# Kernel optimization log

Measured on AMD Instinct MI355X. Metric: run time of the kernel, lower is better.

Reference implementation:

```python
import jax, jax.numpy as jnp
import numpy as np

DIM = 64      # d_model, expand=1 -> d_inner = DIM
H_IN = 128
W_IN = 128
DS = 8        # d_state
DTR = 4       # dt_rank = ceil(DIM/16)
DCONV = 4     # conv kernel size
NDIR = 4      # bimamba v6: h-fwd, h-bwd, w-fwd, w-bwd


def layernorm(x, g, b, eps=1e-5):
    m = x.mean(-1, keepdims=True)
    v = x.var(-1, keepdims=True)
    return (x - m) / jnp.sqrt(v + eps) * g + b


def causal_conv(x, w, b):
    # x: (B, L, D), w: (D, 1, K) depthwise, causal left pad
    xt = x.transpose(0, 2, 1)  # (B, D, L)
    y = jax.lax.conv_general_dilated(xt, w, (1,), [(DCONV - 1, 0)],
                                     feature_group_count=xt.shape[1])
    return y.transpose(0, 2, 1) + b


def selective_scan(u, delta, A, Bm, Cm, D):
    # u,delta: (B,L,D); A: (D,N); Bm,Cm: (B,L,N); D: (D,)
    dA = jnp.exp(delta[..., None] * A)                       # (B,L,D,N)
    dBu = delta[..., None] * Bm[:, :, None, :] * u[..., None]

    def comb(c1, c2):
        a1, b1 = c1
        a2, b2 = c2
        return a1 * a2, a2 * b1 + b2

    _, hs = jax.lax.associative_scan(comb, (dA, dBu), axis=1)  # (B,L,D,N)
    return jnp.einsum('bldn,bln->bld', hs, Cm) + u * D


def setup_inputs() -> dict:
    key = jax.random.key(0)
    ks = jax.random.split(key, 12)
    s = 0.02
    inp = {
        'input': jax.random.normal(ks[0], (2, DIM, H_IN, W_IN), jnp.float32),
        'ln_g': jnp.ones((DIM,), jnp.float32),
        'ln_b': jnp.zeros((DIM,), jnp.float32),
        'in_proj_w': jax.random.normal(ks[1], (2 * DIM, DIM), jnp.float32) * s,
        'conv_w': jax.random.normal(ks[2], (NDIR, DIM, 1, DCONV), jnp.float32) * s,
        'conv_b': jnp.zeros((NDIR, DIM), jnp.float32),
        'xproj_w': jax.random.normal(ks[3], (NDIR, DTR + 2 * DS, DIM), jnp.float32) * s,
        'dtproj_w': jax.random.normal(ks[4], (NDIR, DIM, DTR), jnp.float32) * s,
        'dtproj_b': jax.random.normal(ks[5], (NDIR, DIM), jnp.float32) * 0.1,
        'A_log': jnp.broadcast_to(jnp.log(jnp.arange(1.0, DS + 1.0, dtype=jnp.float32)),
                                  (NDIR, DIM, DS)).copy(),
        'D_skip': jnp.ones((NDIR, DIM), jnp.float32),
        'on_g': jnp.ones((DIM,), jnp.float32),
        'on_b': jnp.zeros((DIM,), jnp.float32),
        'out_proj_w': jax.random.normal(ks[6], (DIM, DIM), jnp.float32) * s,
    }
    return inp


def reference(input, ln_g, ln_b, in_proj_w, conv_w, conv_b, xproj_w,
              dtproj_w, dtproj_b, A_log, D_skip, on_g, on_b, out_proj_w):
    B, C, H, W = input.shape
    L = H * W
    seq = input.reshape(B, C, L).transpose(0, 2, 1)           # b (h w) c
    seq = layernorm(seq, ln_g, ln_b)
    xz = seq @ in_proj_w.T                                    # (B,L,2D)
    x, z = jnp.split(xz, 2, axis=-1)

    ar = jnp.arange(L)
    perm = (ar % H) * W + ar // H    # (h w) -> (w h)
    inv = (ar % W) * H + ar // W     # (w h) -> (h w)

    dirs = [(None, False), (None, True), (perm, False), (perm, True)]
    y_sum = jnp.zeros_like(x)
    for i, (p, rev) in enumerate(dirs):
        xd = x if p is None else x[:, p]
        if rev:
            xd = jnp.flip(xd, 1)
        xd = jax.nn.silu(causal_conv(xd, conv_w[i], conv_b[i]))
        dbl = xd @ xproj_w[i].T
        dt, Bm, Cm = jnp.split(dbl, [DTR, DTR + DS], axis=-1)
        dt = jax.nn.softplus(dt @ dtproj_w[i].T + dtproj_b[i])
        A = -jnp.exp(A_log[i])
        yd = selective_scan(xd, dt, A, Bm, Cm, D_skip[i])
        if rev:
            yd = jnp.flip(yd, 1)
        if p is not None:
            yd = yd[:, inv]
        y_sum = y_sum + yd

    y = y_sum / float(NDIR)                 # if_devide_out=True
    y = layernorm(y, on_g, on_b)            # use_norm=True
    y = y * jax.nn.silu(z)                  # gate
    out = y @ out_proj_w.T
    return out.transpose(0, 2, 1).reshape(B, C, H, W) + input
```

## Files before the change

### kernel.cpp

```cpp
#include <hip/hip_runtime.h>
#include <hip/hip_bf16.h>
#include <cstdint>
#include <cstddef>

#define L_TOT 16384
#define B_SZ 2
#define NROW (B_SZ * L_TOT)
#define CHUNK 32
#define NCH (L_TOT / CHUNK)

static constexpr size_t SLOT_XD  = (size_t)NROW * 64;
static constexpr size_t SLOT_DBC = (size_t)NROW * 20;
static constexpr size_t SLOT_SDT = (size_t)B_SZ * 64 * NCH;
static constexpr size_t SLOT_HC  = (size_t)B_SZ * NCH * 64 * 8;

__device__ __forceinline__ int tau_map(int dir, int s) {
  int j = (dir & 1) ? (L_TOT - 1 - s) : s;
  if (dir >= 2) j = ((j & 127) << 7) | (j >> 7);
  return j;
}
__device__ __forceinline__ float silu_f(float x) { return x / (1.f + __expf(-x)); }
__device__ __forceinline__ float softplus_f(float x) {
  return fmaxf(x, 0.f) + __logf(1.f + __expf(-fabsf(x)));
}

__global__ void __launch_bounds__(256)
k_ln_inproj(const float* __restrict__ inp, const float* __restrict__ lng,
            const float* __restrict__ lnb, const float* __restrict__ W,
            float* __restrict__ xout, float* __restrict__ zout) {
  __shared__ float xt[64 * 65];
  __shared__ float wrk[8448];
  const int t = threadIdx.x;
  const int lane = t & 63;
  const int w = t >> 6;
  const int b = blockIdx.x >> 8;
  const int l0 = (blockIdx.x & 255) << 6;
  const float* ip = inp + (size_t)b * 64 * L_TOT + l0 + lane;
#pragma unroll 4
  for (int cc = 0; cc < 16; ++cc) {
    int c = cc * 4 + w;
    xt[lane * 65 + c] = ip[(size_t)c * L_TOT];
  }
  __syncthreads();
  {
    float s1 = 0.f, s2 = 0.f;
    const int c0 = w * 16;
#pragma unroll
    for (int cc = 0; cc < 16; ++cc) {
      float v = xt[lane * 65 + c0 + cc];
      s1 += v; s2 = fmaf(v, v, s2);
    }
    wrk[w * 64 + lane] = s1;
    wrk[256 + w * 64 + lane] = s2;
  }
  __syncthreads();
  if (t < 64) {
    float s1 = wrk[t] + wrk[64 + t] + wrk[128 + t] + wrk[192 + t];
    float s2 = wrk[256 + t] + wrk[320 + t] + wrk[384 + t] + wrk[448 + t];
    float m = s1 * 0.015625f;
    float var = s2 * 0.015625f - m * m;
    wrk[512 + t] = m;
    wrk[576 + t] = rsqrtf(var + 1e-5f);
  }
  __syncthreads();
  {
    const float mv = wrk[512 + lane], rv = wrk[576 + lane];
#pragma unroll 4
    for (int k = 0; k < 16; ++k) {
      int c = w + 4 * k;
      float g = lng[c], bb = lnb[c];
      float v = xt[lane * 65 + c];
      xt[lane * 65 + c] = (v - mv) * rv * g + bb;
    }
  }
  __syncthreads();
#pragma unroll 4
  for (int rep = 0; rep < 32; ++rep) {
    int j = rep * 4 + w;
    wrk[j * 65 + lane] = W[(size_t)j * 64 + lane];
  }
  __syncthreads();
  const int rg = lane & 15;
  const int jg = lane >> 4;
  const int j0 = w * 32 + jg * 8;
  const int r0 = rg * 4;
  float acc[4][8] = {};
#pragma unroll 2
  for (int c = 0; c < 64; ++c) {
    float xv[4], wv[8];
#pragma unroll
    for (int i = 0; i < 4; ++i) xv[i] = xt[(r0 + i) * 65 + c];
#pragma unroll
    for (int jj = 0; jj < 8; ++jj) wv[jj] = wrk[(j0 + jj) * 65 + c];
#pragma unroll
    for (int i = 0; i < 4; ++i)
#pragma unroll
      for (int jj = 0; jj < 8; ++jj) acc[i][jj] = fmaf(xv[i], wv[jj], acc[i][jj]);
  }
  __syncthreads();
#pragma unroll
  for (int i = 0; i < 4; ++i)
#pragma unroll
    for (int jj = 0; jj < 8; ++jj) wrk[(r0 + i) * 132 + j0 + jj] = acc[i][jj];
  __syncthreads();
  float* xo = xout + ((size_t)b * L_TOT + l0) * 64;
  float* zo = zout + ((size_t)b * L_TOT + l0) * 64;
#pragma unroll 4
  for (int rep = 0; rep < 16; ++rep) {
    int r = rep * 4 + w;
    xo[(size_t)r * 64 + lane] = wrk[r * 132 + lane];
    zo[(size_t)r * 64 + lane] = wrk[r * 132 + 64 + lane];
  }
}

__global__ void __launch_bounds__(256)
k_convproj(const float* __restrict__ xbuf, const float* __restrict__ cw,
           const float* __restrict__ cb, const float* __restrict__ xpw,
           float* __restrict__ xd_base, float* __restrict__ dbc_base,
           int dir_base) {
  __shared__ float xh[67 * 65];
  __shared__ float wt[20 * 65];
  __shared__ float dbl[64 * 20];
  const int t = threadIdx.x;
  const int lane = t & 63;
  const int w = t >> 6;
  const int slot = blockIdx.y;
  const int dir = dir_base + slot;
  const int blk = blockIdx.x;
  const int b = blk >> 8;
  const int s0 = (blk & 255) << 6;
  const float* xb = xbuf + (size_t)b * L_TOT * 64;
#pragma unroll 1
  for (int i = w; i < 67; i += 4) {
    int s = s0 - 3 + i;
    float v = 0.f;
    if (s >= 0) v = xb[(size_t)tau_map(dir, s) * 64 + lane];
    xh[i * 65 + lane] = v;
  }
#pragma unroll
  for (int jj = 0; jj < 5; ++jj) {
    int j = jj * 4 + w;
    wt[j * 65 + lane] = xpw[((size_t)dir * 20 + j) * 64 + lane];
  }
  __syncthreads();
  float wk[4];
#pragma unroll
  for (int k = 0; k < 4; ++k) wk[k] = cw[(dir * 64 + lane) * 4 + k];
  const float bconv = cb[dir * 64 + lane];
  float u[16];
  float* xdp = xd_base + (size_t)slot * SLOT_XD + ((size_t)b * L_TOT + s0) * 64;
#pragma unroll 4
  for (int rr = 0; rr < 16; ++rr) {
    const int r = rr * 4 + w;
    float acc = bconv;
#pragma unroll
    for (int k = 0; k < 4; ++k) acc = fmaf(wk[k], xh[(r + k) * 65 + lane], acc);
    acc = silu_f(acc);
    u[rr] = acc;
    xdp[(size_t)r * 64 + lane] = acc;
  }
  __syncthreads();
  float* xt = xh;
#pragma unroll 4
  for (int rr = 0; rr < 16; ++rr) xt[(rr * 4 + w) * 65 + lane] = u[rr];
  __syncthreads();
  {
    float acc5[5] = {0.f, 0.f, 0.f, 0.f, 0.f};
#pragma unroll 2
    for (int c = 0; c < 64; ++c) {
      float xv = xt[lane * 65 + c];
#pragma unroll
      for (int jj = 0; jj < 5; ++jj)
        acc5[jj] = fmaf(xv, wt[(w * 5 + jj) * 65 + c], acc5[jj]);
    }
#pragma unroll
    for (int jj = 0; jj < 5; ++jj) dbl[lane * 20 + w * 5 + jj] = acc5[jj];
  }
  __syncthreads();
  float* dbp = dbc_base + (size_t)slot * SLOT_DBC + ((size_t)b * L_TOT + s0) * 20;
#pragma unroll
  for (int i = t; i < 1280; i += 256) dbp[i] = dbl[i];
}

__global__ void __launch_bounds__(256, 4)
k_scan1(const float* __restrict__ xd_base, const float* __restrict__ dbc_base,
        const float* __restrict__ alog, const float* __restrict__ dtw,
        const float* __restrict__ dtbias,
        float* __restrict__ hcb, float* __restrict__ sdtb, int dir_base) {
  __shared__ float rpl[4 * CHUNK * 20];
  const int t = threadIdx.x;
  const int w = t >> 6;
  const int d = t & 63;
  const int ch = blockIdx.x * 4 + w;
  const int slot = blockIdx.y;
  const int dir = dir_base + slot;
  const int b = blockIdx.z;
  const float* rblk = dbc_base + (size_t)slot * SLOT_DBC +
                      ((size_t)b * L_TOT + (size_t)blockIdx.x * 4 * CHUNK) * 20;
#pragma unroll 1
  for (int i = t; i < 4 * CHUNK * 20; i += 256) rpl[i] = rblk[i];
  __syncthreads();
  const float* rp = rpl + w * CHUNK * 20;
  float a[8];
#pragma unroll
  for (int n = 0; n < 8; ++n) a[n] = -__expf(alog[((size_t)dir * 64 + d) * 8 + n]);
  float wdt[4];
#pragma unroll
  for (int r = 0; r < 4; ++r) wdt[r] = dtw[((size_t)dir * 64 + d) * 4 + r];
  const float bia = dtbias[dir * 64 + d];
  const float* up = xd_base + (size_t)slot * SLOT_XD + ((size_t)b * L_TOT + ch * CHUNK) * 64;
  float h[8] = {0,0,0,0,0,0,0,0};
  float sdt = 0.f;
#pragma unroll 4
  for (int s = 0; s < CHUNK; ++s) {
    float u = up[s * 64 + d];
    float dt = bia;
#pragma unroll
    for (int r = 0; r < 4; ++r) dt = fmaf(rp[s * 20 + r], wdt[r], dt);
    dt = softplus_f(dt);
    sdt += dt;
    float du = dt * u;
#pragma unroll
    for (int n = 0; n < 8; ++n)
      h[n] = fmaf(__expf(dt * a[n]), h[n], du * rp[s * 20 + 4 + n]);
  }
  sdtb[(size_t)slot * SLOT_SDT + (((size_t)b * 64 + d) * NCH) + ch] = sdt;
  float* hp = hcb + (size_t)slot * SLOT_HC + (((size_t)b * NCH + ch) * 64 + d) * 8;
#pragma unroll
  for (int n = 0; n < 8; ++n) hp[n] = h[n];
}

__global__ void k_scan2(float* __restrict__ hcb, const float* __restrict__ sdtb,
                        const float* __restrict__ alog, int dir_base) {
  const int t = threadIdx.x;
  const int d = blockIdx.x >> 3;
  const int n = blockIdx.x & 7;
  const int slot = blockIdx.y;
  const int dir = dir_base + slot;
  const int b = blockIdx.z;
  const float a = -__expf(alog[((size_t)dir * 64 + d) * 8 + n]);
  float* hcp = hcb + (size_t)slot * SLOT_HC + (size_t)b * NCH * 512;
  const float* sdp = sdtb + (size_t)slot * SLOT_SDT + ((size_t)b * 64 + d) * NCH;
  float e = __expf(a * sdp[t]);
  float v = hcp[((size_t)t * 64 + d) * 8 + n];
  __shared__ float sE[NCH], sV[NCH];
  sE[t] = e; sV[t] = v;
  __syncthreads();
#pragma unroll
  for (int off = 1; off < NCH; off <<= 1) {
    float pe = 1.f, pv = 0.f;
    if (t >= off) { pe = sE[t - off]; pv = sV[t - off]; }
    __syncthreads();
    v = fmaf(e, pv, v);
    e = e * pe;
    sE[t] = e; sV[t] = v;
    __syncthreads();
  }
  const float hs = (t == 0) ? 0.f : sV[t - 1];
  hcp[((size_t)t * 64 + d) * 8 + n] = hs;
}

__global__ void __launch_bounds__(256, 4)
k_scan3(const float* xd_in, const float* __restrict__ dbc_base,
        const float* __restrict__ hcb, const float* __restrict__ alog,
        const float* __restrict__ dtw, const float* __restrict__ dtbias,
        const float* __restrict__ dsk, float* y_base,
        int dir_base, int scatter) {
  __shared__ float rpl[4 * CHUNK * 20];
  const int t = threadIdx.x;
  const int w = t >> 6;
  const int d = t & 63;
  const int ch = blockIdx.x * 4 + w;
  const int slot = blockIdx.y;
  const int dir = dir_base + slot;
  const int b = blockIdx.z;
  const float* rblk = dbc_base + (size_t)slot * SLOT_DBC +
                      ((size_t)b * L_TOT + (size_t)blockIdx.x * 4 * CHUNK) * 20;
#pragma unroll 1
  for (int i = t; i < 4 * CHUNK * 20; i += 256) rpl[i] = rblk[i];
  __syncthreads();
  const float* rp = rpl + w * CHUNK * 20;
  float a[8];
#pragma unroll
  for (int n = 0; n < 8; ++n) a[n] = -__expf(alog[((size_t)dir * 64 + d) * 8 + n]);
  float wdt[4];
#pragma unroll
  for (int r = 0; r < 4; ++r) wdt[r] = dtw[((size_t)dir * 64 + d) * 4 + r];
  const float bia = dtbias[dir * 64 + d];
  const float Dv = dsk[dir * 64 + d];
  const float* up = xd_in + (size_t)slot * SLOT_XD + ((size_t)b * L_TOT + ch * CHUNK) * 64;
  const float* hsp = hcb + (size_t)slot * SLOT_HC + (((size_t)b * NCH + ch) * 64 + d) * 8;
  float h[8];
#pragma unroll
  for (int n = 0; n < 8; ++n) h[n] = hsp[n];
  const int sbase = ch * CHUNK;
#pragma unroll 4
  for (int s = 0; s < CHUNK; ++s) {
    float u = up[s * 64 + d];
    float dt = bia;
#pragma unroll
    for (int r = 0; r < 4; ++r) dt = fmaf(rp[s * 20 + r], wdt[r], dt);
    dt = softplus_f(dt);
    float du = dt * u;
    float y = u * Dv;
#pragma unroll
    for (int n = 0; n < 8; ++n) {
      h[n] = fmaf(__expf(dt * a[n]), h[n], du * rp[s * 20 + 4 + n]);
      y = fmaf(rp[s * 20 + 12 + n], h[n], y);
    }
    if (scatter) {
      int l = tau_map(dir, sbase + s);
      float* yp = y_base + ((size_t)b * L_TOT + l) * 64 + d;
      *yp += y;
    } else {
      y_base[(size_t)slot * SLOT_XD + ((size_t)b * L_TOT + sbase + s) * 64 + d] = y;
    }
  }
}

__global__ void __launch_bounds__(256)
k_final(const float* __restrict__ ybase, const float* __restrict__ zbuf,
        const float* __restrict__ ong, const float* __restrict__ onb,
        const float* __restrict__ OW, const float* __restrict__ inp,
        float* __restrict__ out, int gather) {
  __shared__ float xt[64 * 65];
  __shared__ float tzw[64 * 65];
  __shared__ float st[640];
  const int t = threadIdx.x;
  const int lane = t & 63;
  const int w = t >> 6;
  const int b = blockIdx.x >> 8;
  const int l0 = (blockIdx.x & 255) << 6;
#pragma unroll 2
  for (int rep = 0; rep < 16; ++rep) {
    int r = rep * 4 + w;
    int l = l0 + r;
    float acc;
    if (gather) {
      acc = 0.f;
#pragma unroll
      for (int dir = 0; dir < 4; ++dir) {
        int s = tau_map(dir, l);
        acc += ybase[(size_t)dir * SLOT_XD + ((size_t)b * L_TOT + s) * 64 + lane];
      }
    } else {
      acc = ybase[((size_t)b * L_TOT + l) * 64 + lane];
    }
    xt[r * 65 + lane] = acc * 0.25f;
    tzw[r * 65 + lane] = zbuf[((size_t)b * L_TOT + l) * 64 + lane];
  }
  __syncthreads();
  {
    float s1 = 0.f, s2 = 0.f;
    const int c0 = w * 16;
#pragma unroll
    for (int cc = 0; cc < 16; ++cc) {
      float v = xt[lane * 65 + c0 + cc];
      s1 += v; s2 = fmaf(v, v, s2);
    }
    st[w * 64 + lane] = s1;
    st[256 + w * 64 + lane] = s2;
  }
  __syncthreads();
  if (t < 64) {
    float s1 = st[t] + st[64 + t] + st[128 + t] + st[192 + t];
    float s2 = st[256 + t] + st[320 + t] + st[384 + t] + st[448 + t];
    float m = s1 * 0.015625f;
    float var = s2 * 0.015625f - m * m;
    st[512 + t] = m;
    st[576 + t] = rsqrtf(var + 1e-5f);
  }
  __syncthreads();
  {
    const float mv = st[512 + lane], rv = st[576 + lane];
#pragma unroll 4
    for (int k = 0; k < 16; ++k) {
      int c = w + 4 * k;
      float g = ong[c], bb = onb[c];
      float v = xt[lane * 65 + c];
      float zz = tzw[lane * 65 + c];
      xt[lane * 65 + c] = ((v - mv) * rv * g + bb) * silu_f(zz);
    }
  }
  __syncthreads();
#pragma unroll 4
  for (int rep = 0; rep < 16; ++rep) {
    int j = rep * 4 + w;
    tzw[j * 65 + lane] = OW[(size_t)j * 64 + lane];
  }
  __syncthreads();
  const int rg = lane & 15;
  const int jg = lane >> 4;
  const int j0 = w * 16 + jg * 4;
  const int r0 = rg * 4;
  float acc[4][4] = {};
#pragma unroll 2
  for (int c = 0; c < 64; ++c) {
    float xv[4], wv[4];
#pragma unroll
    for (int i = 0; i < 4; ++i) xv[i] = xt[(r0 + i) * 65 + c];
#pragma unroll
    for (int jj = 0; jj < 4; ++jj) wv[jj] = tzw[(j0 + jj) * 65 + c];
#pragma unroll
    for (int i = 0; i < 4; ++i)
#pragma unroll
      for (int jj = 0; jj < 4; ++jj) acc[i][jj] = fmaf(xv[i], wv[jj], acc[i][jj]);
  }
  __syncthreads();
#pragma unroll
  for (int i = 0; i < 4; ++i)
#pragma unroll
    for (int jj = 0; jj < 4; ++jj) xt[(j0 + jj) * 65 + r0 + i] = acc[i][jj];
  __syncthreads();
#pragma unroll 4
  for (int rep = 0; rep < 16; ++rep) {
    int j = rep * 4 + w;
    size_t o = ((size_t)b * 64 + j) * L_TOT + l0 + lane;
    out[o] = xt[j * 65 + lane] + inp[o];
  }
}

extern "C" void kernel_launch(void* const* d_in, const int* in_sizes, int n_in,
                              void* d_out, int out_size, void* d_ws, size_t ws_size,
                              hipStream_t stream) {
  const float* inp    = (const float*)d_in[0];
  const float* lng    = (const float*)d_in[1];
  const float* lnb    = (const float*)d_in[2];
  const float* ipw    = (const float*)d_in[3];
  const float* cw     = (const float*)d_in[4];
  const float* cb     = (const float*)d_in[5];
  const float* xpw    = (const float*)d_in[6];
  const float* dtw    = (const float*)d_in[7];
  const float* dtbias = (const float*)d_in[8];
  const float* alog   = (const float*)d_in[9];
  const float* dsk    = (const float*)d_in[10];
  const float* ong    = (const float*)d_in[11];
  const float* onb    = (const float*)d_in[12];
  const float* opw    = (const float*)d_in[13];
  float* out = (float*)d_out;
  float* ws = (float*)d_ws;

  const size_t need_batched = (6 * SLOT_XD + 4 * SLOT_DBC + 4 * SLOT_SDT) * sizeof(float);

  if (ws_size >= need_batched) {
    size_t off = 0;
    float* xbuf = ws + off; off += SLOT_XD;
    float* zbuf = ws + off; off += SLOT_XD;
    float* xd   = ws + off; off += 4 * SLOT_XD;
    float* dbc  = ws + off; off += 4 * SLOT_DBC;
    float* sdt  = ws + off; off += 4 * SLOT_SDT;
    float* hc   = xbuf;

    k_ln_inproj<<<dim3(512), 256, 0, stream>>>(inp, lng, lnb, ipw, xbuf, zbuf);
    k_convproj<<<dim3(512, 4), 256, 0, stream>>>(xbuf, cw, cb, xpw, xd, dbc, 0);
    k_scan1<<<dim3(NCH / 4, 4, B_SZ), 256, 0, stream>>>(xd, dbc, alog, dtw, dtbias, hc, sdt, 0);
    k_scan2<<<dim3(512, 4, B_SZ), NCH, 0, stream>>>(hc, sdt, alog, 0);
    k_scan3<<<dim3(NCH / 4, 4, B_SZ), 256, 0, stream>>>(xd, dbc, hc, alog, dtw, dtbias, dsk,
                                                        xd, 0, 0);
    k_final<<<dim3(512), 256, 0, stream>>>(xd, zbuf, ong, onb, opw, inp, out, 1);
  } else {
    size_t off = 0;
    float* xbuf = ws + off; off += SLOT_XD;
    float* zbuf = ws + off; off += SLOT_XD;
    float* ysum = ws + off; off += SLOT_XD;
    float* xd   = ws + off; off += SLOT_XD;
    float* dbc  = ws + off; off += SLOT_DBC;
    float* sdt  = ws + off; off += SLOT_SDT;
    float* hc   = ws + off; off += SLOT_HC;

    hipMemsetAsync(ysum, 0, SLOT_XD * sizeof(float), stream);
    k_ln_inproj<<<dim3(512), 256, 0, stream>>>(inp, lng, lnb, ipw, xbuf, zbuf);
    for (int d2 = 0; d2 < 4; ++d2) {
      k_convproj<<<dim3(512, 1), 256, 0, stream>>>(xbuf, cw, cb, xpw, xd, dbc, d2);
      k_scan1<<<dim3(NCH / 4, 1, B_SZ), 256, 0, stream>>>(xd, dbc, alog, dtw, dtbias, hc, sdt, d2);
      k_scan2<<<dim3(512, 1, B_SZ), NCH, 0, stream>>>(hc, sdt, alog, d2);
      k_scan3<<<dim3(NCH / 4, 1, B_SZ), 256, 0, stream>>>(xd, dbc, hc, alog, dtw, dtbias, dsk,
                                                          ysum, d2, 1);
    }
    k_final<<<dim3(512), 256, 0, stream>>>(ysum, zbuf, ong, onb, opw, inp, out, 0);
  }
}
```

Baseline: 152.0 us.

## Halve scan chunk size, store chunk states in fp16, raise occupancy bounds

Shrinks the chunked-scan chunk from 32 to 16 steps, doubling the number of chunks and thus the parallelism in scan1/scan3 and the length of the scan2 inter-chunk prefix (now 1024 threads per block). The inter-chunk hidden states are stored as fp16 half2 pairs to halve their memory traffic, launch bounds are raised to 8 blocks per SM, and the per-chunk loops are fully unrolled. The trade-offs are twice as much chunk-state data, a deeper block-level scan in scan2, and reduced precision in the carried state, which may hurt accuracy.

After: 175.9 us. 1.16x slower.

```diff
diff --git a/kernel.cpp b/kernel.cpp
--- a/kernel.cpp
+++ b/kernel.cpp
@@ -1,12 +1,13 @@
 #include <hip/hip_runtime.h>
 #include <hip/hip_bf16.h>
+#include <hip/hip_fp16.h>
 #include <cstdint>
 #include <cstddef>
 
 #define L_TOT 16384
 #define B_SZ 2
 #define NROW (B_SZ * L_TOT)
-#define CHUNK 32
+#define CHUNK 16
 #define NCH (L_TOT / CHUNK)
 
 static constexpr size_t SLOT_XD  = (size_t)NROW * 64;
@@ -182,11 +183,11 @@
   for (int i = t; i < 1280; i += 256) dbp[i] = dbl[i];
 }
 
-__global__ void __launch_bounds__(256, 4)
+__global__ void __launch_bounds__(256, 8)
 k_scan1(const float* __restrict__ xd_base, const float* __restrict__ dbc_base,
         const float* __restrict__ alog, const float* __restrict__ dtw,
         const float* __restrict__ dtbias,
-        float* __restrict__ hcb, float* __restrict__ sdtb, int dir_base) {
+        __half* __restrict__ hcb, float* __restrict__ sdtb, int dir_base) {
   __shared__ float rpl[4 * CHUNK * 20];
   const int t = threadIdx.x;
   const int w = t >> 6;
@@ -211,7 +212,7 @@
   const float* up = xd_base + (size_t)slot * SLOT_XD + ((size_t)b * L_TOT + ch * CHUNK) * 64;
   float h[8] = {0,0,0,0,0,0,0,0};
   float sdt = 0.f;
-#pragma unroll 4
+#pragma unroll
   for (int s = 0; s < CHUNK; ++s) {
     float u = up[s * 64 + d];
     float dt = bia;
@@ -225,13 +226,15 @@
       h[n] = fmaf(__expf(dt * a[n]), h[n], du * rp[s * 20 + 4 + n]);
   }
   sdtb[(size_t)slot * SLOT_SDT + (((size_t)b * 64 + d) * NCH) + ch] = sdt;
-  float* hp = hcb + (size_t)slot * SLOT_HC + (((size_t)b * NCH + ch) * 64 + d) * 8;
-#pragma unroll
-  for (int n = 0; n < 8; ++n) hp[n] = h[n];
-}
-
-__global__ void k_scan2(float* __restrict__ hcb, const float* __restrict__ sdtb,
-                        const float* __restrict__ alog, int dir_base) {
+  __half* hp = hcb + (size_t)slot * SLOT_HC + (((size_t)b * NCH + ch) * 64 + d) * 8;
+#pragma unroll
+  for (int n = 0; n < 8; n += 2)
+    *(__half2*)(hp + n) = __floats2half2_rn(h[n], h[n + 1]);
+}
+
+__global__ void __launch_bounds__(1024)
+k_scan2(__half* __restrict__ hcb, const float* __restrict__ sdtb,
+        const float* __restrict__ alog, int dir_base) {
   const int t = threadIdx.x;
   const int d = blockIdx.x >> 3;
   const int n = blockIdx.x & 7;
@@ -239,10 +242,10 @@
   const int dir = dir_base + slot;
   const int b = blockIdx.z;
   const float a = -__expf(alog[((size_t)dir * 64 + d) * 8 + n]);
-  float* hcp = hcb + (size_t)slot * SLOT_HC + (size_t)b * NCH * 512;
+  __half* hcp = hcb + (size_t)slot * SLOT_HC + (size_t)b * NCH * 512;
   const float* sdp = sdtb + (size_t)slot * SLOT_SDT + ((size_t)b * 64 + d) * NCH;
   float e = __expf(a * sdp[t]);
-  float v = hcp[((size_t)t * 64 + d) * 8 + n];
+  float v = __half2float(hcp[((size_t)t * 64 + d) * 8 + n]);
   __shared__ float sE[NCH], sV[NCH];
   sE[t] = e; sV[t] = v;
   __syncthreads();
@@ -257,12 +260,12 @@
     __syncthreads();
   }
   const float hs = (t == 0) ? 0.f : sV[t - 1];
-  hcp[((size_t)t * 64 + d) * 8 + n] = hs;
-}
-
-__global__ void __launch_bounds__(256, 4)
+  hcp[((size_t)t * 64 + d) * 8 + n] = __float2half(hs);
+}
+
+__global__ void __launch_bounds__(256, 8)
 k_scan3(const float* xd_in, const float* __restrict__ dbc_base,
-        const float* __restrict__ hcb, const float* __restrict__ alog,
+        const __half* __restrict__ hcb, const float* __restrict__ alog,
         const float* __restrict__ dtw, const float* __restrict__ dtbias,
         const float* __restrict__ dsk, float* y_base,
         int dir_base, int scatter) {
@@ -289,12 +292,16 @@
   const float bia = dtbias[dir * 64 + d];
   const float Dv = dsk[dir * 64 + d];
   const float* up = xd_in + (size_t)slot * SLOT_XD + ((size_t)b * L_TOT + ch * CHUNK) * 64;
-  const float* hsp = hcb + (size_t)slot * SLOT_HC + (((size_t)b * NCH + ch) * 64 + d) * 8;
+  const __half* hsp = hcb + (size_t)slot * SLOT_HC + (((size_t)b * NCH + ch) * 64 + d) * 8;
   float h[8];
 #pragma unroll
-  for (int n = 0; n < 8; ++n) h[n] = hsp[n];
+  for (int n = 0; n < 8; n += 2) {
+    __half2 p = *(const __half2*)(hsp + n);
+    h[n] = __low2float(p);
+    h[n + 1] = __high2float(p);
+  }
   const int sbase = ch * CHUNK;
-#pragma unroll 4
+#pragma unroll
   for (int s = 0; s < CHUNK; ++s) {
     float u = up[s * 64 + d];
     float dt = bia;
@@ -449,7 +456,7 @@
     float* xd   = ws + off; off += 4 * SLOT_XD;
     float* dbc  = ws + off; off += 4 * SLOT_DBC;
     float* sdt  = ws + off; off += 4 * SLOT_SDT;
-    float* hc   = xbuf;
+    __half* hc  = (__half*)xbuf;
 
     k_ln_inproj<<<dim3(512), 256, 0, stream>>>(inp, lng, lnb, ipw, xbuf, zbuf);
     k_convproj<<<dim3(512, 4), 256, 0, stream>>>(xbuf, cw, cb, xpw, xd, dbc, 0);
@@ -466,7 +473,7 @@
     float* xd   = ws + off; off += SLOT_XD;
     float* dbc  = ws + off; off += SLOT_DBC;
     float* sdt  = ws + off; off += SLOT_SDT;
-    float* hc   = ws + off; off += SLOT_HC;
+    __half* hc  = (__half*)(ws + off); off += SLOT_HC / 2;
 
     hipMemsetAsync(ysum, 0, SLOT_XD * sizeof(float), stream);
     k_ln_inproj<<<dim3(512), 256, 0, stream>>>(inp, lng, lnb, ipw, xbuf, zbuf);
```

## Fuse chunk-local scan pass into conv/proj kernel and store chunk states in fp16

Applied to the files above, without the earlier changes.

Folds the first scan pass into the conv+x_proj kernel. The per-chunk state and delta sum are computed from the conv output and projections already in shared memory, so the xd and dbc buffers are no longer re-read by a separate kernel launch. The chunk carry states and delta sums are now stored as fp16, with packed 16-byte accesses, to cut traffic for the middle and final scan passes. Only 128 of the 256 threads do the serial scan work, which lengthens that kernel's tail, and fp16 carries reduce precision.

New measurement: 147.3 us. 3.1% less time.

```diff
diff --git a/kernel.cpp b/kernel.cpp
--- a/kernel.cpp
+++ b/kernel.cpp
@@ -1,5 +1,6 @@
 #include <hip/hip_runtime.h>
 #include <hip/hip_bf16.h>
+#include <hip/hip_fp16.h>
 #include <cstdint>
 #include <cstddef>
 
@@ -13,6 +14,8 @@
 static constexpr size_t SLOT_DBC = (size_t)NROW * 20;
 static constexpr size_t SLOT_SDT = (size_t)B_SZ * 64 * NCH;
 static constexpr size_t SLOT_HC  = (size_t)B_SZ * NCH * 64 * 8;
+
+union H8pack { float4 f4; __half2 h2[4]; };
 
 __device__ __forceinline__ int tau_map(int dir, int s) {
   int j = (dir & 1) ? (L_TOT - 1 - s) : s;
@@ -114,10 +117,12 @@
 }
 
 __global__ void __launch_bounds__(256)
-k_convproj(const float* __restrict__ xbuf, const float* __restrict__ cw,
+k_convscan(const float* __restrict__ xbuf, const float* __restrict__ cw,
            const float* __restrict__ cb, const float* __restrict__ xpw,
+           const float* __restrict__ dtw, const float* __restrict__ dtbias,
+           const float* __restrict__ alog,
            float* __restrict__ xd_base, float* __restrict__ dbc_base,
-           int dir_base) {
+           __half* __restrict__ hcb, __half* __restrict__ sdtb, int dir_base) {
   __shared__ float xh[67 * 65];
   __shared__ float wt[20 * 65];
   __shared__ float dbl[64 * 20];
@@ -180,58 +185,45 @@
   float* dbp = dbc_base + (size_t)slot * SLOT_DBC + ((size_t)b * L_TOT + s0) * 20;
 #pragma unroll
   for (int i = t; i < 1280; i += 256) dbp[i] = dbl[i];
-}
-
-__global__ void __launch_bounds__(256, 4)
-k_scan1(const float* __restrict__ xd_base, const float* __restrict__ dbc_base,
-        const float* __restrict__ alog, const float* __restrict__ dtw,
-        const float* __restrict__ dtbias,
-        float* __restrict__ hcb, float* __restrict__ sdtb, int dir_base) {
-  __shared__ float rpl[4 * CHUNK * 20];
-  const int t = threadIdx.x;
-  const int w = t >> 6;
-  const int d = t & 63;
-  const int ch = blockIdx.x * 4 + w;
-  const int slot = blockIdx.y;
-  const int dir = dir_base + slot;
-  const int b = blockIdx.z;
-  const float* rblk = dbc_base + (size_t)slot * SLOT_DBC +
-                      ((size_t)b * L_TOT + (size_t)blockIdx.x * 4 * CHUNK) * 20;
-#pragma unroll 1
-  for (int i = t; i < 4 * CHUNK * 20; i += 256) rpl[i] = rblk[i];
-  __syncthreads();
-  const float* rp = rpl + w * CHUNK * 20;
-  float a[8];
-#pragma unroll
-  for (int n = 0; n < 8; ++n) a[n] = -__expf(alog[((size_t)dir * 64 + d) * 8 + n]);
-  float wdt[4];
-#pragma unroll
-  for (int r = 0; r < 4; ++r) wdt[r] = dtw[((size_t)dir * 64 + d) * 4 + r];
-  const float bia = dtbias[dir * 64 + d];
-  const float* up = xd_base + (size_t)slot * SLOT_XD + ((size_t)b * L_TOT + ch * CHUNK) * 64;
-  float h[8] = {0,0,0,0,0,0,0,0};
-  float sdt = 0.f;
-#pragma unroll 4
-  for (int s = 0; s < CHUNK; ++s) {
-    float u = up[s * 64 + d];
-    float dt = bia;
-#pragma unroll
-    for (int r = 0; r < 4; ++r) dt = fmaf(rp[s * 20 + r], wdt[r], dt);
-    dt = softplus_f(dt);
-    sdt += dt;
-    float du = dt * u;
-#pragma unroll
-    for (int n = 0; n < 8; ++n)
-      h[n] = fmaf(__expf(dt * a[n]), h[n], du * rp[s * 20 + 4 + n]);
-  }
-  sdtb[(size_t)slot * SLOT_SDT + (((size_t)b * 64 + d) * NCH) + ch] = sdt;
-  float* hp = hcb + (size_t)slot * SLOT_HC + (((size_t)b * NCH + ch) * 64 + d) * 8;
-#pragma unroll
-  for (int n = 0; n < 8; ++n) hp[n] = h[n];
-}
-
-__global__ void k_scan2(float* __restrict__ hcb, const float* __restrict__ sdtb,
-                        const float* __restrict__ alog, int dir_base) {
+  if (t < 128) {
+    const int w2 = t >> 6;
+    const int d = t & 63;
+    const int ch = (s0 >> 5) + w2;
+    float a[8];
+#pragma unroll
+    for (int n = 0; n < 8; ++n) a[n] = -__expf(alog[((size_t)dir * 64 + d) * 8 + n]);
+    float wdt[4];
+#pragma unroll
+    for (int r = 0; r < 4; ++r) wdt[r] = dtw[((size_t)dir * 64 + d) * 4 + r];
+    const float bia = dtbias[dir * 64 + d];
+    const float* xs = xt + (w2 * 32) * 65;
+    const float* ds = dbl + (w2 * 32) * 20;
+    float h[8] = {0,0,0,0,0,0,0,0};
+    float sdt = 0.f;
+#pragma unroll 4
+    for (int s = 0; s < CHUNK; ++s) {
+      float uu = xs[s * 65 + d];
+      float dt = bia;
+#pragma unroll
+      for (int r = 0; r < 4; ++r) dt = fmaf(ds[s * 20 + r], wdt[r], dt);
+      dt = softplus_f(dt);
+      sdt += dt;
+      float du = dt * uu;
+#pragma unroll
+      for (int n = 0; n < 8; ++n)
+        h[n] = fmaf(__expf(dt * a[n]), h[n], du * ds[s * 20 + 4 + n]);
+    }
+    sdtb[(size_t)slot * SLOT_SDT + ((size_t)b * 64 + d) * NCH + ch] = __float2half(sdt);
+    H8pack pk;
+#pragma unroll
+    for (int k = 0; k < 4; ++k) pk.h2[k] = __floats2half2_rn(h[2 * k], h[2 * k + 1]);
+    *(float4*)(hcb + (size_t)slot * SLOT_HC + (((size_t)b * NCH + ch) * 64 + d) * 8) = pk.f4;
+  }
+}
+
+__global__ void __launch_bounds__(512)
+k_scan2(__half* __restrict__ hcb, const __half* __restrict__ sdtb,
+        const float* __restrict__ alog, int dir_base) {
   const int t = threadIdx.x;
   const int d = blockIdx.x >> 3;
   const int n = blockIdx.x & 7;
@@ -239,10 +231,10 @@
   const int dir = dir_base + slot;
   const int b = blockIdx.z;
   const float a = -__expf(alog[((size_t)dir * 64 + d) * 8 + n]);
-  float* hcp = hcb + (size_t)slot * SLOT_HC + (size_t)b * NCH * 512;
-  const float* sdp = sdtb + (size_t)slot * SLOT_SDT + ((size_t)b * 64 + d) * NCH;
-  float e = __expf(a * sdp[t]);
-  float v = hcp[((size_t)t * 64 + d) * 8 + n];
+  __half* hcp = hcb + (size_t)slot * SLOT_HC + (size_t)b * NCH * 512;
+  const __half* sdp = sdtb + (size_t)slot * SLOT_SDT + ((size_t)b * 64 + d) * NCH;
+  float e = __expf(a * __half2float(sdp[t]));
+  float v = __half2float(hcp[((size_t)t * 64 + d) * 8 + n]);
   __shared__ float sE[NCH], sV[NCH];
   sE[t] = e; sV[t] = v;
   __syncthreads();
@@ -257,12 +249,12 @@
     __syncthreads();
   }
   const float hs = (t == 0) ? 0.f : sV[t - 1];
-  hcp[((size_t)t * 64 + d) * 8 + n] = hs;
+  hcp[((size_t)t * 64 + d) * 8 + n] = __float2half(hs);
 }
 
 __global__ void __launch_bounds__(256, 4)
 k_scan3(const float* xd_in, const float* __restrict__ dbc_base,
-        const float* __restrict__ hcb, const float* __restrict__ alog,
+        const __half* __restrict__ hcb, const float* __restrict__ alog,
         const float* __restrict__ dtw, const float* __restrict__ dtbias,
         const float* __restrict__ dsk, float* y_base,
         int dir_base, int scatter) {
@@ -289,10 +281,17 @@
   const float bia = dtbias[dir * 64 + d];
   const float Dv = dsk[dir * 64 + d];
   const float* up = xd_in + (size_t)slot * SLOT_XD + ((size_t)b * L_TOT + ch * CHUNK) * 64;
-  const float* hsp = hcb + (size_t)slot * SLOT_HC + (((size_t)b * NCH + ch) * 64 + d) * 8;
   float h[8];
-#pragma unroll
-  for (int n = 0; n < 8; ++n) h[n] = hsp[n];
+  {
+    H8pack pk;
+    pk.f4 = *(const float4*)(hcb + (size_t)slot * SLOT_HC +
+                             (((size_t)b * NCH + ch) * 64 + d) * 8);
+#pragma unroll
+    for (int k = 0; k < 4; ++k) {
+      h[2 * k] = __low2float(pk.h2[k]);
+      h[2 * k + 1] = __high2float(pk.h2[k]);
+    }
+  }
   const int sbase = ch * CHUNK;
 #pragma unroll 4
   for (int s = 0; s < CHUNK; ++s) {
@@ -440,7 +439,8 @@
   float* out = (float*)d_out;
   float* ws = (float*)d_ws;
 
-  const size_t need_batched = (6 * SLOT_XD + 4 * SLOT_DBC + 4 * SLOT_SDT) * sizeof(float);
+  const size_t need_batched = (6 * SLOT_XD + 4 * SLOT_DBC) * sizeof(float) +
+                              (4 * SLOT_SDT + 4 * SLOT_HC) * sizeof(__half);
 
   if (ws_size >= need_batched) {
     size_t off = 0;
@@ -448,12 +448,12 @@
     float* zbuf = ws + off; off += SLOT_XD;
     float* xd   = ws + off; off += 4 * SLOT_XD;
     float* dbc  = ws + off; off += 4 * SLOT_DBC;
-    float* sdt  = ws + off; off += 4 * SLOT_SDT;
-    float* hc   = xbuf;
+    __half* sdt = (__half*)(ws + off); off += (4 * SLOT_SDT) / 2;
+    __half* hc  = (__half*)(ws + off); off += (4 * SLOT_HC) / 2;
 
     k_ln_inproj<<<dim3(512), 256, 0, stream>>>(inp, lng, lnb, ipw, xbuf, zbuf);
-    k_convproj<<<dim3(512, 4), 256, 0, stream>>>(xbuf, cw, cb, xpw, xd, dbc, 0);
-    k_scan1<<<dim3(NCH / 4, 4, B_SZ), 256, 0, stream>>>(xd, dbc, alog, dtw, dtbias, hc, sdt, 0);
+    k_convscan<<<dim3(512, 4), 256, 0, stream>>>(xbuf, cw, cb, xpw, dtw, dtbias, alog,
+                                                 xd, dbc, hc, sdt, 0);
     k_scan2<<<dim3(512, 4, B_SZ), NCH, 0, stream>>>(hc, sdt, alog, 0);
     k_scan3<<<dim3(NCH / 4, 4, B_SZ), 256, 0, stream>>>(xd, dbc, hc, alog, dtw, dtbias, dsk,
                                                         xd, 0, 0);
@@ -465,14 +465,14 @@
     float* ysum = ws + off; off += SLOT_XD;
     float* xd   = ws + off; off += SLOT_XD;
     float* dbc  = ws + off; off += SLOT_DBC;
-    float* sdt  = ws + off; off += SLOT_SDT;
-    float* hc   = ws + off; off += SLOT_HC;
+    __half* sdt = (__half*)(ws + off); off += SLOT_SDT / 2 + 1;
+    __half* hc  = (__half*)(ws + off); off += SLOT_HC / 2;
 
     hipMemsetAsync(ysum, 0, SLOT_XD * sizeof(float), stream);
     k_ln_inproj<<<dim3(512), 256, 0, stream>>>(inp, lng, lnb, ipw, xbuf, zbuf);
     for (int d2 = 0; d2 < 4; ++d2) {
-      k_convproj<<<dim3(512, 1), 256, 0, stream>>>(xbuf, cw, cb, xpw, xd, dbc, d2);
-      k_scan1<<<dim3(NCH / 4, 1, B_SZ), 256, 0, stream>>>(xd, dbc, alog, dtw, dtbias, hc, sdt, d2);
+      k_convscan<<<dim3(512, 1), 256, 0, stream>>>(xbuf, cw, cb, xpw, dtw, dtbias, alog,
+                                                   xd, dbc, hc, sdt, d2);
       k_scan2<<<dim3(512, 1, B_SZ), NCH, 0, stream>>>(hc, sdt, alog, d2);
       k_scan3<<<dim3(NCH / 4, 1, B_SZ), 256, 0, stream>>>(xd, dbc, hc, alog, dtw, dtbias, dsk,
                                                           ysum, d2, 1);
```
